# Kernel tuning notes

Hardware: AMD Instinct MI355X
Metric: run time of the kernel (lower is better)

The kernel has to match this reference:

```python
import jax, jax.numpy as jnp
import numpy as np

LAMBDA_COORD = 5.0
LAMBDA_NOOBJ = 0.5
B, N, F = 2048, 64, 19  # batch, nb_pred, 2 + n_classes


def _greedy_scan(Permut, v, h, D2, mask, n):
    # One greedy-assignment phase: n sequential argmax/one-hot steps.
    def step(carry, _):
        Permut, v, h, D2 = carry
        D2 = D2 * v[:, :, None] * h[:, None, :]
        A = jax.nn.one_hot(jnp.argmax(D2, axis=-1), n, dtype=D2.dtype)          # row-wise best col
        Bm = v[:, :, None] * A * D2
        C = jnp.swapaxes(jax.nn.one_hot(jnp.argmax(Bm, axis=-2), n, dtype=D2.dtype), -1, -2)  # col-wise best row
        E = v[:, :, None] * A * C
        Permut = Permut + E
        v = (1.0 - Permut.sum(-1)) * mask
        h = 1.0 - Permut.sum(-2)
        return (Permut, v, h, D2), None
    (Permut, v, h, D2), _ = jax.lax.scan(step, (Permut, v, h, D2), None, length=n)
    return Permut, v, h, D2


def _permute_ypred(y_true, y_pred):
    alpha = y_true[:, :, 0]                      # [B, N] in {0,1}
    x = y_true[:, :, 1]
    p = y_pred[:, :, 1]
    n = x.shape[-1]
    D1 = 1.0 - jnp.abs(x[:, :, None] - p[:, None, :])   # [B, N, N] similarity

    # Phase 1: match ground-truth positives (rows with alpha=1).
    Permut0 = jnp.zeros_like(D1)
    v0 = alpha
    h0 = jnp.ones_like(alpha)
    D2_0 = v0[:, :, None] * D1
    Permut, v, h, _ = _greedy_scan(Permut0, v0, h0, D2_0, alpha, n)

    # Phase 2: match remaining rows (alpha=0) to remaining predictions.
    neg = 1.0 - alpha
    D2_1 = neg[:, :, None] * D1 * h[:, None, :]
    Permut, _, _, _ = _greedy_scan(Permut, neg, h, D2_1, neg, n)

    permutation = jnp.argmax(Permut, axis=-1)            # [B, N]
    idx = jnp.broadcast_to(permutation[:, :, None], y_pred.shape)
    return jnp.take_along_axis(y_pred, idx, axis=1)


def setup_inputs() -> dict:
    key = jax.random.key(0)
    k1, k2, k3 = jax.random.split(key, 3)
    y_true = jax.random.uniform(k1, (B, N, F), dtype=jnp.float32)
    alpha = (jax.random.uniform(k3, (B, N)) < 0.3).astype(jnp.float32)
    y_true = y_true.at[:, :, 0].set(alpha)
    y_pred = jax.random.uniform(k2, (B, N, F), dtype=jnp.float32)
    return {"y_true": y_true, "y_pred": y_pred}


def reference(y_true, y_pred):
    y_pred = _permute_ypred(y_true, y_pred)
    a = y_true[:, :, 0]
    loss = jnp.sum(
        a * LAMBDA_COORD * jnp.square(y_true[:, :, 1] - y_pred[:, :, 1])
        + a * jnp.square(a - y_pred[:, :, 0])
        + (1.0 - a) * LAMBDA_NOOBJ * jnp.square(a - y_pred[:, :, 0])
        + a * jnp.sum(jnp.square(y_true[:, :, 2:] - y_pred[:, :, 2:]), axis=-1)
    )
    return loss
```

## Files before the change

### kernel.cpp

```cpp
#include <hip/hip_runtime.h>
#include <stdint.h>


#define NN 64
#define NF 19

__global__ __launch_bounds__(64) void spotting_loss_kernel(
    const float* __restrict__ yt, const float* __restrict__ yp,
    float* __restrict__ out)
{
  const int b = blockIdx.x;
  const int i = threadIdx.x;
  const float* __restrict__ ytb = yt + (size_t)b * NN * NF;
  const float* __restrict__ ypb = yp + (size_t)b * NN * NF;

  __shared__ float p_sh[NN];
  __shared__ unsigned long long key_sh[NN];

  const float alpha = ytb[i * NF + 0];
  const float x     = ytb[i * NF + 1];
  p_sh[i] = ypb[i * NF + 1];
  __syncthreads();

  float D1r[NN];
#pragma unroll
  for (int j = 0; j < NN; ++j) {
    D1r[j] = 1.0f - fabsf(x - p_sh[j]);
  }

  unsigned long long hbits = ~0ull;
  int   perm  = 0;
  int   jmax  = 0;
  float best  = 0.0f;

  for (int phase = 0; phase < 2; ++phase) {
    bool vlive  = (phase == 0) ? (alpha > 0.5f) : (alpha < 0.5f);
    bool rescan = vlive;

    for (int it = 0; it < NN; ++it) {
      if (__ballot(vlive) == 0ull) break;

      if (rescan) {
        const unsigned hlo = (unsigned)hbits;
        const unsigned hhi = (unsigned)(hbits >> 32);
        best = -1.0f; jmax = 0;
#pragma unroll
        for (int j = 0; j < NN; ++j) {
          const unsigned bit = (j < 32) ? ((hlo >> j) & 1u)
                                        : ((hhi >> (j - 32)) & 1u);
          const unsigned msk = 0u - bit;
          const float t = __uint_as_float(__float_as_uint(D1r[j]) & msk);
          if (t > best) { best = t; jmax = j; }
        }
        rescan = false;
      }

      key_sh[i] = 63ull;
      __syncthreads();

      if (vlive && best > 0.0f) {
        const unsigned long long key =
            (((unsigned long long)__float_as_uint(best)) << 6) |
            (unsigned long long)(63 - i);
        atomicMax(&key_sh[jmax], key);
      }
      __syncthreads();

      const unsigned long long kc = key_sh[i];
      const bool colkill = (kc >> 6) != 0ull;
      const unsigned long long killed = __ballot(colkill);

      if (vlive) {
        const unsigned long long kw = key_sh[jmax];
        const int winner = 63 - (int)(kw & 63ull);
        if (winner == i) {
          perm = jmax;
          vlive = false;
        } else if ((killed >> jmax) & 1ull) {
          rescan = true;
        }
      }
      hbits &= ~killed;
      __syncthreads();
    }
  }

  const float* __restrict__ ypr = ypb + (size_t)perm * NF;
  const float a  = alpha;
  const float p0 = ypr[0];
  const float p1 = ypr[1];
  const float dx = x - p1;
  const float da = a - p0;
  float s2 = 0.0f;
#pragma unroll
  for (int f = 2; f < NF; ++f) {
    const float d = ytb[i * NF + f] - ypr[f];
    s2 += d * d;
  }
  float l = a * 5.0f * (dx * dx)
          + a * (da * da)
          + (1.0f - a) * 0.5f * (da * da)
          + a * s2;

#pragma unroll
  for (int off = 32; off > 0; off >>= 1) l += __shfl_down(l, off);
  if (i == 0) atomicAdd(out, l);
}

extern "C" void kernel_launch(void* const* d_in, const int* in_sizes, int n_in,
                              void* d_out, int out_size, void* d_ws, size_t ws_size,
                              hipStream_t stream) {
  const float* yt = (const float*)d_in[0];
  const float* yp = (const float*)d_in[1];
  float* out = (float*)d_out;
  const int B = in_sizes[0] / (NN * NF);

  hipMemsetAsync(out, 0, sizeof(float) * (size_t)out_size, stream);
  spotting_loss_kernel<<<B, 64, 0, stream>>>(yt, yp, out);
}
```

Before: 105.7 us.

## Presort per-row column preferences with bitonic sort and walk pointer instead of rescanning

Each row now bitonic-sorts its 64 similarity keys in registers once and stores the column order as packed bytes in shared memory. In each greedy step the row advances a pointer to its next column that is still free, replacing the repeated masked argmax over 64 values. The per-iteration reset of the column keys and one barrier are dropped, since the columns that stay claimed are already masked out through hbits. The trade is a large fixed sorting cost per thread and higher register pressure (a 64-entry u64 array), and launch bounds now request 2 blocks per CU.

```diff
diff --git a/kernel.cpp b/kernel.cpp
--- a/kernel.cpp
+++ b/kernel.cpp
@@ -4,8 +4,9 @@
 
 #define NN 64
 #define NF 19
+typedef unsigned long long u64;
 
-__global__ __launch_bounds__(64) void spotting_loss_kernel(
+__global__ __launch_bounds__(64, 2) void spotting_loss_kernel(
     const float* __restrict__ yt, const float* __restrict__ yp,
     float* __restrict__ out)
 {
@@ -15,69 +16,91 @@
   const float* __restrict__ ypb = yp + (size_t)b * NN * NF;
 
   __shared__ float p_sh[NN];
-  __shared__ unsigned long long key_sh[NN];
+  __shared__ u64 key_sh[NN];
+  __shared__ unsigned int pref[NN][17];
 
   const float alpha = ytb[i * NF + 0];
   const float x     = ytb[i * NF + 1];
-  p_sh[i] = ypb[i * NF + 1];
+  p_sh[i]   = ypb[i * NF + 1];
+  key_sh[i] = 63ull;
   __syncthreads();
 
-  float D1r[NN];
+  u64 k[NN];
 #pragma unroll
   for (int j = 0; j < NN; ++j) {
-    D1r[j] = 1.0f - fabsf(x - p_sh[j]);
+    const float d = 1.0f - fabsf(x - p_sh[j]);
+    k[j] = (((u64)(0x40000000u - __float_as_uint(d))) << 6) | (u64)j;
   }
 
-  unsigned long long hbits = ~0ull;
-  int   perm  = 0;
-  int   jmax  = 0;
-  float best  = 0.0f;
+#pragma unroll
+  for (int sz = 2; sz <= NN; sz <<= 1) {
+#pragma unroll
+    for (int st = sz >> 1; st > 0; st >>= 1) {
+#pragma unroll
+      for (int t = 0; t < NN; ++t) {
+        const int u = t ^ st;
+        if (u > t) {
+          const bool up = ((t & sz) == 0);
+          const u64 a = k[t], c2 = k[u];
+          const bool sw = up ? (a > c2) : (a < c2);
+          k[t] = sw ? c2 : a;
+          k[u] = sw ? a : c2;
+        }
+      }
+    }
+  }
 
+#pragma unroll
+  for (int r = 0; r < NN; r += 4) {
+    pref[i][r >> 2] = (unsigned)(k[r] & 63ull)
+                    | ((unsigned)(k[r + 1] & 63ull) << 8)
+                    | ((unsigned)(k[r + 2] & 63ull) << 16)
+                    | ((unsigned)(k[r + 3] & 63ull) << 24);
+  }
+
+  const unsigned int* __restrict__ prow = &pref[i][0];
+  u64 hbits = ~0ull;
+  int perm  = 0;
+  int ptr   = 0;
+  int wptr  = -1;
+  unsigned win = 0;
+
+#pragma unroll 1
   for (int phase = 0; phase < 2; ++phase) {
-    bool vlive  = (phase == 0) ? (alpha > 0.5f) : (alpha < 0.5f);
-    bool rescan = vlive;
+    bool vlive = (phase == 0) ? (alpha > 0.5f) : (alpha < 0.5f);
 
+#pragma unroll 1
     for (int it = 0; it < NN; ++it) {
       if (__ballot(vlive) == 0ull) break;
 
-      if (rescan) {
-        const unsigned hlo = (unsigned)hbits;
-        const unsigned hhi = (unsigned)(hbits >> 32);
-        best = -1.0f; jmax = 0;
-#pragma unroll
-        for (int j = 0; j < NN; ++j) {
-          const unsigned bit = (j < 32) ? ((hlo >> j) & 1u)
-                                        : ((hhi >> (j - 32)) & 1u);
-          const unsigned msk = 0u - bit;
-          const float t = __uint_as_float(__float_as_uint(D1r[j]) & msk);
-          if (t > best) { best = t; jmax = j; }
+      int  c = 0;
+      bool found = false;
+      if (vlive) {
+        while (ptr < NN) {
+          const int wi = ptr >> 2;
+          if (wi != wptr) { win = prow[wi]; wptr = wi; }
+          const int cc = (win >> ((ptr & 3) * 8)) & 63;
+          if ((hbits >> cc) & 1ull) { c = cc; found = true; break; }
+          ++ptr;
         }
-        rescan = false;
-      }
-
-      key_sh[i] = 63ull;
-      __syncthreads();
-
-      if (vlive && best > 0.0f) {
-        const unsigned long long key =
-            (((unsigned long long)__float_as_uint(best)) << 6) |
-            (unsigned long long)(63 - i);
-        atomicMax(&key_sh[jmax], key);
+        if (found) {
+          const float val = 1.0f - fabsf(x - p_sh[c]);
+          const u64 key = (((u64)__float_as_uint(val)) << 6) |
+                          (u64)(63 - i);
+          atomicMax(&key_sh[c], key);
+        }
       }
       __syncthreads();
 
-      const unsigned long long kc = key_sh[i];
+      const u64 kc = key_sh[i];
       const bool colkill = (kc >> 6) != 0ull;
-      const unsigned long long killed = __ballot(colkill);
+      const u64 killed = __ballot(colkill);
 
-      if (vlive) {
-        const unsigned long long kw = key_sh[jmax];
-        const int winner = 63 - (int)(kw & 63ull);
-        if (winner == i) {
-          perm = jmax;
+      if (found) {
+        const u64 kw = key_sh[c];
+        if ((int)(kw & 63ull) == 63 - i) {
+          perm  = c;
           vlive = false;
-        } else if ((killed >> jmax) & 1ull) {
-          rescan = true;
         }
       }
       hbits &= ~killed;
```

Measured after the change: 111.8 us. +5.8%, slower.
